# Optimization experiments

Hardware: AMD Instinct MI355X
Metric: run time of the kernel (lower is better)

Reference implementation:

```python
import jax, jax.numpy as jnp
import numpy as np

B, S, D = 4, 2048, 768
LN_EPS = 1e-12


def setup_inputs() -> dict:
    key = jax.random.key(0)
    k0, k1, k2, k3 = jax.random.split(key, 4)
    scale = 1.0 / np.sqrt(D).astype(np.float32)
    return {
        "hidden_states": jax.random.normal(k0, (B, S, D), jnp.float32),
        "attention_mask": jnp.ones((B, 1, S, S), jnp.int32),
        "prior_n_attn": jax.random.uniform(k1, (B, S, S), jnp.float32),
        "ln_w": jnp.ones((D,), jnp.float32),
        "ln_b": jnp.zeros((D,), jnp.float32),
        "wq": jax.random.normal(k2, (D, D), jnp.float32) * scale,
        "bq": jnp.zeros((D,), jnp.float32),
        "wk": jax.random.normal(k3, (D, D), jnp.float32) * scale,
        "bk": jnp.zeros((D,), jnp.float32),
    }


def reference(hidden_states, attention_mask, prior_n_attn, ln_w, ln_b, wq, bq, wk, bk):
    _, S_, D_ = hidden_states.shape
    # LayerNorm (biased variance, as torch.nn.LayerNorm)
    mu = hidden_states.mean(-1, keepdims=True)
    var = ((hidden_states - mu) ** 2).mean(-1, keepdims=True)
    h = (hidden_states - mu) / jnp.sqrt(var + LN_EPS) * ln_w + ln_b

    a = jnp.eye(S_, k=1, dtype=jnp.int32)      # superdiagonal
    bI = jnp.eye(S_, dtype=jnp.int32)          # diagonal
    c = jnp.eye(S_, k=-1, dtype=jnp.int32)     # subdiagonal
    tri = jnp.triu(jnp.ones((S_, S_), jnp.float32))

    # mask & (a + c): band of width 1 off the diagonal; then squeeze dim 1
    mask = (attention_mask.astype(jnp.int32) & (a + c))[:, 0]  # [B,S,S]

    q = h @ wq + bq
    k = h @ wk + bk
    scores = jnp.einsum("bsd,btd->bst", q, k) / D_
    scores = jnp.where(mask == 0, -jnp.inf, scores)
    n = jnp.nan_to_num(jax.nn.softmax(scores, axis=-1))
    n = jnp.sqrt(n * jnp.swapaxes(n, -2, -1) + 1e-9)
    n = prior_n_attn + (1.0 - prior_n_attn) * n

    # keep only the superdiagonal of log(n + 1e-9); zero elsewhere
    logm = jnp.log(n + 1e-9) * a.astype(n.dtype)
    # prefix-sum via triangular matmuls (same math as torch source)
    t = logm @ tri                                   # [B,S,S]
    g = jnp.exp(jnp.einsum("ij,bjk->bik", tri, t))   # [B,S,S]
    su = tri - bI.astype(tri.dtype)                  # strictly-upper indicator
    g = g * su                                       # masked_fill((tri-b)==0, 0)
    diag_part = jnp.where(bI == 0, 1e-9, n)          # n.masked_fill(b==0, 1e-9)
    g = g + jnp.swapaxes(g, -2, -1) + diag_part
    return (g, n)
```

## Files before the change

kernel.cpp:

```cpp
#include <hip/hip_runtime.h>
#include <hip/hip_bf16.h>
#include <math.h>
#include <stdint.h>

#define BB 4
#define SS 2048
#define DD 768
#define MM (BB*SS)

typedef __attribute__((ext_vector_type(4))) float  f32x4;
typedef __attribute__((ext_vector_type(8))) __bf16 bf16x8;
typedef __attribute__((ext_vector_type(4))) __bf16 bf16x4;

#define AS1 __attribute__((address_space(1)))
#define AS3 __attribute__((address_space(3)))

__global__ __launch_bounds__(256) void combined_kernel(
        const float* __restrict__ x, const float* __restrict__ lw,
        const float* __restrict__ lb, const float* __restrict__ wq,
        const float* __restrict__ wk, const float* __restrict__ bq,
        const float* __restrict__ bk, const int* __restrict__ att,
        const float* __restrict__ prior, __bf16* __restrict__ G,
        float* __restrict__ u, float* __restrict__ v, float* __restrict__ cb,
        __bf16* __restrict__ h, int* __restrict__ fl, float* __restrict__ prsup,
        float* __restrict__ du_g, float* __restrict__ dn_g, float* __restrict__ w_g) {
    __shared__ __attribute__((aligned(16))) __bf16 As[64][32];
    __shared__ __attribute__((aligned(16))) __bf16 Bs[64][32];
    const int bid = blockIdx.x;
    if (bid >= 2577) {
        const int idx = (bid - 2577) * 256 + threadIdx.x;
        const int b = idx >> 11, s = idx & 2047;
        const bool au = (s < SS - 1) && ((att[((size_t)b * SS + s) * SS + (s + 1)] & 1) != 0);
        const bool ad = (s > 0)      && ((att[((size_t)b * SS + s) * SS + (s - 1)] & 1) != 0);
        fl[idx] = (au ? 1 : 0) | (ad ? 2 : 0);
        if (s < SS - 1)
            prsup[idx] = prior[((size_t)b * SS + s) * SS + s + 1];
        du_g[idx] = 0.f; dn_g[idx] = 0.f; w_g[idx] = 0.f;
        return;
    }
    if (bid >= 529) {
        const int row = (bid - 529) * 4 + (threadIdx.x >> 6);
        const int lane = threadIdx.x & 63;
        const float* xr = x + (size_t)row * DD + lane * 12;
        f32x4 a0 = *(const f32x4*)(xr), a1 = *(const f32x4*)(xr + 4), a2 = *(const f32x4*)(xr + 8);
        float xs[12];
#pragma unroll
        for (int c = 0; c < 4; c++) { xs[c] = a0[c]; xs[4 + c] = a1[c]; xs[8 + c] = a2[c]; }
        float s = 0.f, ss = 0.f;
#pragma unroll
        for (int c = 0; c < 12; c++) { s += xs[c]; ss += xs[c] * xs[c]; }
#pragma unroll
        for (int o = 1; o < 64; o <<= 1) { s += __shfl_xor(s, o); ss += __shfl_xor(ss, o); }
        const float mu = s * (1.0f / DD);
        const float var = ss * (1.0f / DD) - mu * mu;
        const float rstd = 1.0f / sqrtf(var + 1e-12f);
        const float* wp = lw + lane * 12; const float* bp = lb + lane * 12;
        f32x4 w0 = *(const f32x4*)(wp), w1 = *(const f32x4*)(wp + 4), w2 = *(const f32x4*)(wp + 8);
        f32x4 b0 = *(const f32x4*)(bp), b1 = *(const f32x4*)(bp + 4), b2 = *(const f32x4*)(bp + 8);
        bf16x4 o0, o1, o2;
#pragma unroll
        for (int c = 0; c < 4; c++) {
            o0[c] = (__bf16)((xs[c]     - mu) * rstd * w0[c] + b0[c]);
            o1[c] = (__bf16)((xs[4 + c] - mu) * rstd * w1[c] + b1[c]);
            o2[c] = (__bf16)((xs[8 + c] - mu) * rstd * w2[c] + b2[c]);
        }
        __bf16* hr = h + (size_t)row * DD + lane * 12;
        *(bf16x4*)(hr) = o0; *(bf16x4*)(hr + 4) = o1; *(bf16x4*)(hr + 8) = o2;
        return;
    }
    if (bid >= 144) {
        const int id = bid - 144;
        const int lane = threadIdx.x & 63, wv_ = threadIdx.x >> 6;
        if (id == 384) {
            if (wv_ != 0) return;
            float s = 0.f;
#pragma unroll
            for (int m = 0; m < 12; m++) s += bq[lane + 64 * m] * bk[lane + 64 * m];
#pragma unroll
            for (int o = 1; o < 64; o <<= 1) s += __shfl_xor(s, o);
            if (lane == 0) cb[0] = s;
            return;
        }
        const bool isU = id < 192;
        const int row = (isU ? id : id - 192) * 4 + wv_;
        const float* W = isU ? wq : wk;
        const float* bvec = isU ? bk : bq;
        const float* wr_ = W + (size_t)row * DD;
        float s = 0.f;
#pragma unroll
        for (int m = 0; m < 12; m++) s += wr_[lane + 64 * m] * bvec[lane + 64 * m];
#pragma unroll
        for (int o = 1; o < 64; o <<= 1) s += __shfl_xor(s, o);
        if (lane == 0) (isU ? u : v)[row] = s;
        return;
    }
    const int m0 = (bid % 12) * 64;
    const int n0 = (bid / 12) * 64;
    const int t = threadIdx.x;
    const int wave = t >> 6, lane = t & 63;
    const int wr = wave >> 1, wc = wave & 1;
    const int srow = t >> 2, scol = (t & 3) * 8;
    f32x4 acc[2][2] = {};

    for (int k0 = 0; k0 < DD; k0 += 32) {
        const float* ga = wq + (size_t)(m0 + srow) * DD + k0 + scol;
        const float* gb = wk + (size_t)(n0 + srow) * DD + k0 + scol;
        f32x4 a0 = *(const f32x4*)(ga), a1 = *(const f32x4*)(ga + 4);
        f32x4 b0 = *(const f32x4*)(gb), b1 = *(const f32x4*)(gb + 4);
        bf16x8 av, bv;
#pragma unroll
        for (int c = 0; c < 4; c++) {
            av[c] = (__bf16)a0[c]; av[4 + c] = (__bf16)a1[c];
            bv[c] = (__bf16)b0[c]; bv[4 + c] = (__bf16)b1[c];
        }
        __syncthreads();
        *(bf16x8*)&As[srow][scol] = av;
        *(bf16x8*)&Bs[srow][scol] = bv;
        __syncthreads();
        const int r = lane & 15, ko = (lane >> 4) << 3;
        bf16x8 af[2], bvf[2];
#pragma unroll
        for (int i = 0; i < 2; i++) af[i]  = *(const bf16x8*)&As[wr * 32 + i * 16 + r][ko];
#pragma unroll
        for (int j = 0; j < 2; j++) bvf[j] = *(const bf16x8*)&Bs[wc * 32 + j * 16 + r][ko];
#pragma unroll
        for (int i = 0; i < 2; i++)
#pragma unroll
            for (int j = 0; j < 2; j++)
                acc[i][j] = __builtin_amdgcn_mfma_f32_16x16x32_bf16(af[i], bvf[j], acc[i][j], 0, 0, 0);
    }
#pragma unroll
    for (int i = 0; i < 2; i++) {
        const int mm = m0 + wr * 32 + i * 16 + (lane >> 4) * 4;
#pragma unroll
        for (int j = 0; j < 2; j++) {
            const int nn = n0 + wc * 32 + j * 16 + (lane & 15);
#pragma unroll
            for (int rr = 0; rr < 4; rr++)
                G[(size_t)(mm + rr) * DD + nn] = (__bf16)acc[i][j][rr];
        }
    }
}

__global__ __launch_bounds__(256) void rgemm_kernel(const __bf16* __restrict__ A,
        const __bf16* __restrict__ Bt, const float* __restrict__ u,
        const float* __restrict__ v, float* __restrict__ du_g,
        float* __restrict__ dn_g, float* __restrict__ w_g) {
    __shared__ __attribute__((aligned(16))) __bf16 As[64 * 32];
    __shared__ __attribute__((aligned(16))) __bf16 Bs[128 * 32];
    const int bid = blockIdx.x;
    const int mt = bid & 127, nt = bid >> 7;
    const int m0 = mt * 64, n0 = nt * 128;
    const int t = threadIdx.x;
    const int wave = t >> 6, lane = t & 63;
    const int wr = wave >> 1, wc = wave & 1;
    f32x4 acc[2][4] = {};

    char* asb = (char*)As;
    char* bsb = (char*)Bs;
    const int rloc = lane >> 2;
    const int slot = lane & 3;
    const int rA = wave * 16 + rloc;
    const int csw = (slot ^ ((rA >> 1) & 3)) << 3;

    for (int k0 = 0; k0 < DD; k0 += 32) {
        const __bf16* ga  = A  + (size_t)(m0 + rA) * DD + k0 + csw;
        const __bf16* gb0 = Bt + (size_t)(n0 + rA) * DD + k0 + csw;
        const __bf16* gb1 = gb0 + (size_t)64 * DD;
        __builtin_amdgcn_global_load_lds((const AS1 void*)(ga),  (AS3 void*)(asb + wave * 1024),        16, 0, 0);
        __builtin_amdgcn_global_load_lds((const AS1 void*)(gb0), (AS3 void*)(bsb + wave * 1024),        16, 0, 0);
        __builtin_amdgcn_global_load_lds((const AS1 void*)(gb1), (AS3 void*)(bsb + 4096 + wave * 1024), 16, 0, 0);
        __syncthreads();
        const int r = lane & 15, ks = lane >> 4;
        bf16x8 af[2], bvf[4];
#pragma unroll
        for (int i = 0; i < 2; i++) {
            const int R = wr * 32 + i * 16 + r;
            af[i] = *(const bf16x8*)&As[R * 32 + ((ks ^ ((R >> 1) & 3)) << 3)];
        }
#pragma unroll
        for (int j = 0; j < 4; j++) {
            const int R = wc * 64 + j * 16 + r;
            bvf[j] = *(const bf16x8*)&Bs[R * 32 + ((ks ^ ((R >> 1) & 3)) << 3)];
        }
#pragma unroll
        for (int i = 0; i < 2; i++)
#pragma unroll
            for (int j = 0; j < 4; j++)
                acc[i][j] = __builtin_amdgcn_mfma_f32_16x16x32_bf16(af[i], bvf[j], acc[i][j], 0, 0, 0);
        __syncthreads();
    }
    int colg[4]; float ub[4], vb[4];
#pragma unroll
    for (int j = 0; j < 4; j++) {
        colg[j] = n0 + wc * 64 + j * 16 + (lane & 15);
        ub[j] = u[colg[j]];
        vb[j] = v[colg[j]];
    }
#pragma unroll
    for (int i = 0; i < 2; i++) {
#pragma unroll
        for (int rr = 0; rr < 4; rr++) {
            const int row = m0 + wr * 32 + i * 16 + (lane >> 4) * 4 + rr;
            const int rm = (row == 0) ? 0 : row - 1;
            const int rp = (row == MM - 1) ? MM - 1 : row + 1;
            const __bf16* hm = A + (size_t)rm * DD;
            const __bf16* hz = A + (size_t)row * DD;
            const __bf16* hp = A + (size_t)rp * DD;
            float dua = 0.f, dna = 0.f, wa = 0.f;
#pragma unroll
            for (int j = 0; j < 4; j++) {
                const float Rv = acc[i][j][rr] + ub[j];
                dua += Rv * (float)hm[colg[j]];
                dna += Rv * (float)hp[colg[j]];
                wa  += vb[j] * (float)hz[colg[j]];
            }
#pragma unroll
            for (int o = 1; o < 16; o <<= 1) {
                dua += __shfl_xor(dua, o);
                dna += __shfl_xor(dna, o);
                wa  += __shfl_xor(wa, o);
            }
            if ((lane & 15) == 0) {
                atomicAdd(&du_g[row], dua);
                atomicAdd(&dn_g[row], dna);
                atomicAdd(&w_g[row], wa);
            }
        }
    }
}

__global__ __launch_bounds__(256) void scan_kernel(const float* __restrict__ du_g,
        const float* __restrict__ dn_g, const float* __restrict__ w_g,
        const float* __restrict__ cbp, const int* __restrict__ fl_i,
        const float* __restrict__ prsup,
        float* __restrict__ nb, double* __restrict__ P2) {
    const int b = blockIdx.x;
    const int t = threadIdx.x;
    __shared__ float du_s[SS], dn_s[SS], w_s[SS], sh_pd[SS];
    __shared__ double warr[256];
    for (int x = t; x < SS; x += 256) {
        du_s[x] = du_g[b * SS + x];
        dn_s[x] = dn_g[b * SS + x];
        w_s[x]  = w_g[b * SS + x];
    }
    __syncthreads();
    const float cb = cbp[0];
    float pu_r[8];
#pragma unroll
    for (int e = 0; e < 8; e++) {
        const int s = t * 8 + e;
        const int fl = fl_i[b * SS + s];
        const bool au = fl & 1, ad = fl & 2;
        float puv = 0.f, pdv = 0.f;
        if (au || ad) {
            const float eu = au ? (du_s[s + 1] + w_s[s + 1] + cb) * (1.0f / DD) : 0.f;
            const float ed = ad ? (dn_s[s - 1] + w_s[s - 1] + cb) * (1.0f / DD) : 0.f;
            float mx = au ? eu : ed;
            if (au && ad) mx = fmaxf(eu, ed);
            const float zu = au ? expf(eu - mx) : 0.f;
            const float zd = ad ? expf(ed - mx) : 0.f;
            const float iz = 1.f / (zu + zd);
            puv = zu * iz; pdv = zd * iz;
        }
        pu_r[e] = puv;
        sh_pd[s] = pdv;
    }
    __syncthreads();
    double L[8];
    double mysum = 0.0;
#pragma unroll
    for (int e = 0; e < 8; e++) {
        const int s = t * 8 + e;
        double Lv = 0.0;
        float nbv = 0.f;
        if (s < SS - 1) {
            nbv = sqrtf(pu_r[e] * sh_pd[s + 1] + 1e-9f);
            const float pr = prsup[b * SS + s];
            const float nsup = pr + (1.f - pr) * nbv;
            Lv = (double)log2f(nsup + 1e-9f);
        }
        nb[b * SS + s] = nbv;
        L[e] = Lv; mysum += Lv;
    }
    warr[t] = mysum;
    __syncthreads();
    for (int o = 1; o < 256; o <<= 1) {
        double vv = 0.0;
        if (t >= o) vv = warr[t - o];
        __syncthreads();
        if (t >= o) warr[t] += vv;
        __syncthreads();
    }
    double run = warr[t] - mysum;
#pragma unroll
    for (int e = 0; e < 8; e++) {
        P2[(size_t)b * SS + t * 8 + e] = run;
        run += L[e];
    }
}

__global__ __launch_bounds__(256) void out_kernel(const float* __restrict__ prior,
        const float* __restrict__ nb, const double* __restrict__ P2,
        float* __restrict__ gout, float* __restrict__ nout) {
    const size_t t8 = (size_t)blockIdx.x * 256 + threadIdx.x;
    const int b = (int)(t8 >> 19);
    const size_t off = t8 << 3;
    const size_t r = off & ((1u << 22) - 1);
    const int i  = (int)(r >> 11);
    const int k0 = (int)(r & 2047);
    const f32x4 p0 = *(const f32x4*)(prior + off);
    const f32x4 p1 = *(const f32x4*)(prior + off + 4);
    const double* Pb = P2 + ((size_t)b << 11);
    const double Pi = Pb[i];
    const float* nbb = nb + ((size_t)b << 11);
    f32x4 g0, g1, n0, n1;
#pragma unroll
    for (int c = 0; c < 8; c++) {
        const int k = k0 + c;
        const float pr = (c < 4) ? p0[c] : p1[c - 4];
        float vv = 3.16227766016838e-5f;
        if (k == i + 1)      vv = nbb[i];
        else if (k == i - 1) vv = nbb[k];
        const float nval = pr + (1.f - pr) * vv;
        float g;
        if (k == i) {
            g = nval;
        } else {
            const double Pk = Pb[k];
            const double dd = (k > i) ? (Pk - Pi) : (Pi - Pk);
            g = exp2f((float)dd) + 1e-9f;
        }
        if (c < 4) { g0[c] = g; n0[c] = nval; }
        else       { g1[c - 4] = g; n1[c - 4] = nval; }
    }
    *(f32x4*)(gout + off)     = g0;
    *(f32x4*)(gout + off + 4) = g1;
    *(f32x4*)(nout + off)     = n0;
    *(f32x4*)(nout + off + 4) = n1;
}

extern "C" void kernel_launch(void* const* d_in, const int* in_sizes, int n_in,
                              void* d_out, int out_size, void* d_ws, size_t ws_size,
                              hipStream_t stream) {
    const float* hs    = (const float*)d_in[0];
    const int*   att   = (const int*)d_in[1];
    const float* prior = (const float*)d_in[2];
    const float* ln_w  = (const float*)d_in[3];
    const float* ln_b  = (const float*)d_in[4];
    const float* wq    = (const float*)d_in[5];
    const float* bq    = (const float*)d_in[6];
    const float* wk    = (const float*)d_in[7];
    const float* bk    = (const float*)d_in[8];

    float* gout = (float*)d_out;
    float* nout = gout + (size_t)BB * SS * SS;

    char* ws = (char*)d_ws;
    __bf16* h     = (__bf16*)(ws);
    __bf16* G     = (__bf16*)(ws + 12582912);
    float*  u     = (float*) (ws + 13762560);
    float*  v     = (float*) (ws + 13765632);
    float*  cbp   = (float*) (ws + 13768704);
    int*    fl    = (int*)   (ws + 13768960);
    float*  prsup = (float*) (ws + 13801728);
    float*  du_g  = (float*) (ws + 13834496);
    float*  dn_g  = (float*) (ws + 13867264);
    float*  w_g   = (float*) (ws + 13900032);
    float*  nbuf  = (float*) (ws + 13932800);
    double* P2    = (double*)(ws + 13965568);

    combined_kernel<<<dim3(2609), dim3(256), 0, stream>>>(hs, ln_w, ln_b, wq, wk, bq, bk,
                                                          att, prior, G, u, v, cbp, h, fl, prsup,
                                                          du_g, dn_g, w_g);
    rgemm_kernel<<<dim3(768), dim3(256), 0, stream>>>(h, G, u, v, du_g, dn_g, w_g);
    scan_kernel<<<dim3(BB), dim3(256), 0, stream>>>(du_g, dn_g, w_g, cbp, fl, prsup, nbuf, P2);
    out_kernel<<<dim3((BB * SS * SS / 8) / 256), dim3(256), 0, stream>>>(prior, nbuf, P2, gout, nout);
}
```

Baseline: 97.39 us.

## Fuse four kernel launches into one cooperative persistent kernel with grid syncs

Adds a cooperative mega-kernel of 512 blocks that runs the LayerNorm/weight-product prep, the h·G reduction GEMM, the per-batch scan and the output fill in sequence, separated by grid.sync(). It also adds a host-side occupancy check that falls back to the old four-launch path. The intent is to remove three kernel launch gaps and their tail effects. In exchange, the fixed 512-block grid may underuse the GPU in the large output phase, and the scan phase leaves most blocks idle during a grid barrier. The host also now makes device attribute and occupancy queries on every call.

```diff
diff --git a/kernel.cpp b/kernel.cpp
--- a/kernel.cpp
+++ b/kernel.cpp
@@ -1,5 +1,6 @@
 #include <hip/hip_runtime.h>
 #include <hip/hip_bf16.h>
+#include <hip/hip_cooperative_groups.h>
 #include <math.h>
 #include <stdint.h>
 
@@ -7,6 +8,7 @@
 #define SS 2048
 #define DD 768
 #define MM (BB*SS)
+#define MGRID 512
 
 typedef __attribute__((ext_vector_type(4))) float  f32x4;
 typedef __attribute__((ext_vector_type(8))) __bf16 bf16x8;
@@ -14,6 +16,330 @@
 
 #define AS1 __attribute__((address_space(1)))
 #define AS3 __attribute__((address_space(3)))
+
+namespace cg = cooperative_groups;
+
+__global__ __launch_bounds__(256, 2) void mega_kernel(
+        const float* __restrict__ x, const float* __restrict__ lw,
+        const float* __restrict__ lb, const float* __restrict__ wq,
+        const float* __restrict__ bq, const float* __restrict__ wk,
+        const float* __restrict__ bk, const int* __restrict__ att,
+        const float* __restrict__ prior,
+        __bf16* __restrict__ G, float* __restrict__ u, float* __restrict__ v,
+        float* __restrict__ cbp, __bf16* __restrict__ h, int* __restrict__ fl,
+        float* __restrict__ prsup, float* __restrict__ du_g,
+        float* __restrict__ dn_g, float* __restrict__ w_g,
+        float* __restrict__ nbuf, double* __restrict__ P2,
+        float* __restrict__ gout, float* __restrict__ nout) {
+    __shared__ __attribute__((aligned(16))) union {
+        struct { __bf16 As[128 * 32]; __bf16 Bs[96 * 32]; } g;
+        struct { __bf16 As[64][32]; __bf16 Bs[64][32]; } g0;
+        struct { float du[SS], dn[SS], w[SS], pd[SS]; double warr[256]; } s;
+    } sm;
+    cg::grid_group grid = cg::this_grid();
+    const int bid = blockIdx.x;
+    const int t = threadIdx.x;
+    const int wave = t >> 6, lane = t & 63;
+
+    {
+#pragma unroll
+        for (int rr = 0; rr < 4; rr++) {
+            const int row = bid * 16 + wave * 4 + rr;
+            const float* xr = x + (size_t)row * DD + lane * 12;
+            f32x4 a0 = *(const f32x4*)(xr), a1 = *(const f32x4*)(xr + 4), a2 = *(const f32x4*)(xr + 8);
+            float xs[12];
+#pragma unroll
+            for (int c = 0; c < 4; c++) { xs[c] = a0[c]; xs[4 + c] = a1[c]; xs[8 + c] = a2[c]; }
+            float s = 0.f, ss = 0.f;
+#pragma unroll
+            for (int c = 0; c < 12; c++) { s += xs[c]; ss += xs[c] * xs[c]; }
+#pragma unroll
+            for (int o = 1; o < 64; o <<= 1) { s += __shfl_xor(s, o); ss += __shfl_xor(ss, o); }
+            const float mu = s * (1.0f / DD);
+            const float var = ss * (1.0f / DD) - mu * mu;
+            const float rstd = 1.0f / sqrtf(var + 1e-12f);
+            const float* wp = lw + lane * 12; const float* bp = lb + lane * 12;
+            f32x4 w0 = *(const f32x4*)(wp), w1 = *(const f32x4*)(wp + 4), w2 = *(const f32x4*)(wp + 8);
+            f32x4 b0 = *(const f32x4*)(bp), b1 = *(const f32x4*)(bp + 4), b2 = *(const f32x4*)(bp + 8);
+            bf16x4 o0, o1, o2;
+#pragma unroll
+            for (int c = 0; c < 4; c++) {
+                o0[c] = (__bf16)((xs[c]     - mu) * rstd * w0[c] + b0[c]);
+                o1[c] = (__bf16)((xs[4 + c] - mu) * rstd * w1[c] + b1[c]);
+                o2[c] = (__bf16)((xs[8 + c] - mu) * rstd * w2[c] + b2[c]);
+            }
+            __bf16* hr = h + (size_t)row * DD + lane * 12;
+            *(bf16x4*)(hr) = o0; *(bf16x4*)(hr + 4) = o1; *(bf16x4*)(hr + 8) = o2;
+        }
+        if (bid < 144) {
+            const int m0 = (bid % 12) * 64;
+            const int n0 = (bid / 12) * 64;
+            const int wr = wave >> 1, wc = wave & 1;
+            const int srow = t >> 2, scol = (t & 3) * 8;
+            f32x4 acc[2][2] = {};
+            for (int k0 = 0; k0 < DD; k0 += 32) {
+                const float* ga = wq + (size_t)(m0 + srow) * DD + k0 + scol;
+                const float* gb = wk + (size_t)(n0 + srow) * DD + k0 + scol;
+                f32x4 a0 = *(const f32x4*)(ga), a1 = *(const f32x4*)(ga + 4);
+                f32x4 b0 = *(const f32x4*)(gb), b1 = *(const f32x4*)(gb + 4);
+                bf16x8 av, bv;
+#pragma unroll
+                for (int c = 0; c < 4; c++) {
+                    av[c] = (__bf16)a0[c]; av[4 + c] = (__bf16)a1[c];
+                    bv[c] = (__bf16)b0[c]; bv[4 + c] = (__bf16)b1[c];
+                }
+                __syncthreads();
+                *(bf16x8*)&sm.g0.As[srow][scol] = av;
+                *(bf16x8*)&sm.g0.Bs[srow][scol] = bv;
+                __syncthreads();
+                const int r = lane & 15, ko = (lane >> 4) << 3;
+                bf16x8 af[2], bvf[2];
+#pragma unroll
+                for (int i = 0; i < 2; i++) af[i]  = *(const bf16x8*)&sm.g0.As[wr * 32 + i * 16 + r][ko];
+#pragma unroll
+                for (int j = 0; j < 2; j++) bvf[j] = *(const bf16x8*)&sm.g0.Bs[wc * 32 + j * 16 + r][ko];
+#pragma unroll
+                for (int i = 0; i < 2; i++)
+#pragma unroll
+                    for (int j = 0; j < 2; j++)
+                        acc[i][j] = __builtin_amdgcn_mfma_f32_16x16x32_bf16(af[i], bvf[j], acc[i][j], 0, 0, 0);
+            }
+#pragma unroll
+            for (int i = 0; i < 2; i++) {
+                const int mm = m0 + wr * 32 + i * 16 + (lane >> 4) * 4;
+#pragma unroll
+                for (int j = 0; j < 2; j++) {
+                    const int nn = n0 + wc * 32 + j * 16 + (lane & 15);
+#pragma unroll
+                    for (int rr = 0; rr < 4; rr++)
+                        G[(size_t)(mm + rr) * DD + nn] = (__bf16)acc[i][j][rr];
+                }
+            }
+        } else if (bid < 337) {
+            const int base = (bid - 144) * 2;
+#pragma unroll 1
+            for (int q = 0; q < 2; q++) {
+                const int id = base + q;
+                if (id > 384) break;
+                if (id == 384) {
+                    if (wave == 0) {
+                        float s = 0.f;
+#pragma unroll
+                        for (int m = 0; m < 12; m++) s += bq[lane + 64 * m] * bk[lane + 64 * m];
+#pragma unroll
+                        for (int o = 1; o < 64; o <<= 1) s += __shfl_xor(s, o);
+                        if (lane == 0) cbp[0] = s;
+                    }
+                } else {
+                    const bool isU = id < 192;
+                    const int row = (isU ? id : id - 192) * 4 + wave;
+                    const float* W = isU ? wq : wk;
+                    const float* bvec = isU ? bk : bq;
+                    const float* wr_ = W + (size_t)row * DD;
+                    float s = 0.f;
+#pragma unroll
+                    for (int m = 0; m < 12; m++) s += wr_[lane + 64 * m] * bvec[lane + 64 * m];
+#pragma unroll
+                    for (int o = 1; o < 64; o <<= 1) s += __shfl_xor(s, o);
+                    if (lane == 0) (isU ? u : v)[row] = s;
+                }
+            }
+        } else if (bid >= 480) {
+            const int idx = (bid - 480) * 256 + t;
+            const int b = idx >> 11, s = idx & 2047;
+            const bool au = (s < SS - 1) && ((att[((size_t)b * SS + s) * SS + (s + 1)] & 1) != 0);
+            const bool ad = (s > 0)      && ((att[((size_t)b * SS + s) * SS + (s - 1)] & 1) != 0);
+            fl[idx] = (au ? 1 : 0) | (ad ? 2 : 0);
+            if (s < SS - 1)
+                prsup[idx] = prior[((size_t)b * SS + s) * SS + s + 1];
+            du_g[idx] = 0.f; dn_g[idx] = 0.f; w_g[idx] = 0.f;
+        }
+    }
+    grid.sync();
+    {
+        const int mt = bid & 63, nt = bid >> 6;
+        const int m0 = mt * 128, n0 = nt * 96;
+        const int wr = wave >> 1, wc = wave & 1;
+        f32x4 acc[4][3] = {};
+        char* asb = (char*)sm.g.As;
+        char* bsb = (char*)sm.g.Bs;
+        const int rgrp = lane >> 2;
+        const int slot = lane & 3;
+#pragma unroll 1
+        for (int k0 = 0; k0 < DD; k0 += 32) {
+#pragma unroll
+            for (int i2 = 0; i2 < 2; i2++) {
+                const int j = wave * 2 + i2;
+                const int R = j * 16 + rgrp;
+                const int csw = (slot ^ ((R >> 1) & 3)) << 3;
+                __builtin_amdgcn_global_load_lds((const AS1 void*)(h + (size_t)(m0 + R) * DD + k0 + csw),
+                                                 (AS3 void*)(asb + j * 1024), 16, 0, 0);
+                if (j < 6)
+                    __builtin_amdgcn_global_load_lds((const AS1 void*)(G + (size_t)(n0 + R) * DD + k0 + csw),
+                                                     (AS3 void*)(bsb + j * 1024), 16, 0, 0);
+            }
+            __syncthreads();
+            const int r = lane & 15, ks = lane >> 4;
+            bf16x8 af[4], bvf[3];
+#pragma unroll
+            for (int i = 0; i < 4; i++) {
+                const int R = wr * 64 + i * 16 + r;
+                af[i] = *(const bf16x8*)&sm.g.As[R * 32 + ((ks ^ ((R >> 1) & 3)) << 3)];
+            }
+#pragma unroll
+            for (int j = 0; j < 3; j++) {
+                const int R = wc * 48 + j * 16 + r;
+                bvf[j] = *(const bf16x8*)&sm.g.Bs[R * 32 + ((ks ^ ((R >> 1) & 3)) << 3)];
+            }
+#pragma unroll
+            for (int i = 0; i < 4; i++)
+#pragma unroll
+                for (int j = 0; j < 3; j++)
+                    acc[i][j] = __builtin_amdgcn_mfma_f32_16x16x32_bf16(af[i], bvf[j], acc[i][j], 0, 0, 0);
+            __syncthreads();
+        }
+        int colg[3]; float ub[3], vb2[3];
+#pragma unroll
+        for (int j = 0; j < 3; j++) {
+            colg[j] = n0 + wc * 48 + j * 16 + (lane & 15);
+            ub[j] = u[colg[j]];
+            vb2[j] = v[colg[j]];
+        }
+#pragma unroll
+        for (int i = 0; i < 4; i++) {
+#pragma unroll
+            for (int rr = 0; rr < 4; rr++) {
+                const int row = m0 + wr * 64 + i * 16 + (lane >> 4) * 4 + rr;
+                const int rm = (row == 0) ? 0 : row - 1;
+                const int rp = (row == MM - 1) ? MM - 1 : row + 1;
+                const __bf16* hm = h + (size_t)rm * DD;
+                const __bf16* hz = h + (size_t)row * DD;
+                const __bf16* hp = h + (size_t)rp * DD;
+                float dua = 0.f, dna = 0.f, wa = 0.f;
+#pragma unroll
+                for (int j = 0; j < 3; j++) {
+                    const float Rv = acc[i][j][rr] + ub[j];
+                    dua += Rv * (float)hm[colg[j]];
+                    dna += Rv * (float)hp[colg[j]];
+                    wa  += vb2[j] * (float)hz[colg[j]];
+                }
+#pragma unroll
+                for (int o = 1; o < 16; o <<= 1) {
+                    dua += __shfl_xor(dua, o);
+                    dna += __shfl_xor(dna, o);
+                    wa  += __shfl_xor(wa, o);
+                }
+                if ((lane & 15) == 0) {
+                    atomicAdd(&du_g[row], dua);
+                    atomicAdd(&dn_g[row], dna);
+                    atomicAdd(&w_g[row], wa);
+                }
+            }
+        }
+    }
+    grid.sync();
+    if (bid < BB) {
+        const int b = bid;
+        for (int xx = t; xx < SS; xx += 256) {
+            sm.s.du[xx] = du_g[b * SS + xx];
+            sm.s.dn[xx] = dn_g[b * SS + xx];
+            sm.s.w[xx]  = w_g[b * SS + xx];
+        }
+        __syncthreads();
+        const float cb = cbp[0];
+        float pu_r[8];
+#pragma unroll
+        for (int e = 0; e < 8; e++) {
+            const int s = t * 8 + e;
+            const int flg = fl[b * SS + s];
+            const bool au = flg & 1, ad = flg & 2;
+            float puv = 0.f, pdv = 0.f;
+            if (au || ad) {
+                const float eu = au ? (sm.s.du[s + 1] + sm.s.w[s + 1] + cb) * (1.0f / DD) : 0.f;
+                const float ed = ad ? (sm.s.dn[s - 1] + sm.s.w[s - 1] + cb) * (1.0f / DD) : 0.f;
+                float mx = au ? eu : ed;
+                if (au && ad) mx = fmaxf(eu, ed);
+                const float zu = au ? expf(eu - mx) : 0.f;
+                const float zd = ad ? expf(ed - mx) : 0.f;
+                const float iz = 1.f / (zu + zd);
+                puv = zu * iz; pdv = zd * iz;
+            }
+            pu_r[e] = puv;
+            sm.s.pd[s] = pdv;
+        }
+        __syncthreads();
+        double L[8];
+        double mysum = 0.0;
+#pragma unroll
+        for (int e = 0; e < 8; e++) {
+            const int s = t * 8 + e;
+            double Lv = 0.0;
+            float nbv = 0.f;
+            if (s < SS - 1) {
+                nbv = sqrtf(pu_r[e] * sm.s.pd[s + 1] + 1e-9f);
+                const float pr = prsup[b * SS + s];
+                const float nsup = pr + (1.f - pr) * nbv;
+                Lv = (double)log2f(nsup + 1e-9f);
+            }
+            nbuf[b * SS + s] = nbv;
+            L[e] = Lv; mysum += Lv;
+        }
+        sm.s.warr[t] = mysum;
+        __syncthreads();
+        for (int o = 1; o < 256; o <<= 1) {
+            double vv = 0.0;
+            if (t >= o) vv = sm.s.warr[t - o];
+            __syncthreads();
+            if (t >= o) sm.s.warr[t] += vv;
+            __syncthreads();
+        }
+        double run = sm.s.warr[t] - mysum;
+#pragma unroll
+        for (int e = 0; e < 8; e++) {
+            P2[(size_t)b * SS + t * 8 + e] = run;
+            run += L[e];
+        }
+    }
+    grid.sync();
+#pragma unroll 1
+    for (int vb = bid; vb < 8192; vb += MGRID) {
+        const size_t t8 = (size_t)vb * 256 + t;
+        const int b = (int)(t8 >> 19);
+        const size_t off = t8 << 3;
+        const size_t rr_ = off & ((1u << 22) - 1);
+        const int i  = (int)(rr_ >> 11);
+        const int k0 = (int)(rr_ & 2047);
+        const f32x4 p0 = *(const f32x4*)(prior + off);
+        const f32x4 p1 = *(const f32x4*)(prior + off + 4);
+        const double* Pb = P2 + ((size_t)b << 11);
+        const double Pi = Pb[i];
+        const float* nbb = nbuf + ((size_t)b << 11);
+        f32x4 g0, g1, n0v, n1v;
+#pragma unroll
+        for (int c = 0; c < 8; c++) {
+            const int k = k0 + c;
+            const float pr = (c < 4) ? p0[c] : p1[c - 4];
+            float vv = 3.16227766016838e-5f;
+            if (k == i + 1)      vv = nbb[i];
+            else if (k == i - 1) vv = nbb[k];
+            const float nval = pr + (1.f - pr) * vv;
+            float g;
+            if (k == i) {
+                g = nval;
+            } else {
+                const double Pk = Pb[k];
+                const double dd = (k > i) ? (Pk - Pi) : (Pi - Pk);
+                g = exp2f((float)dd) + 1e-9f;
+            }
+            if (c < 4) { g0[c] = g; n0v[c] = nval; }
+            else       { g1[c - 4] = g; n1v[c - 4] = nval; }
+        }
+        *(f32x4*)(gout + off)     = g0;
+        *(f32x4*)(gout + off + 4) = g1;
+        *(f32x4*)(nout + off)     = n0v;
+        *(f32x4*)(nout + off + 4) = n1v;
+    }
+}
 
 __global__ __launch_bounds__(256) void combined_kernel(
         const float* __restrict__ x, const float* __restrict__ lw,
@@ -370,6 +696,30 @@
     float*  nbuf  = (float*) (ws + 13932800);
     double* P2    = (double*)(ws + 13965568);
 
+    bool useCoop = false;
+    {
+        int dev = 0;
+        if (hipGetDevice(&dev) == hipSuccess) {
+            int coop = 0, nCU = 0, maxBlk = 0;
+            hipDeviceGetAttribute(&coop, hipDeviceAttributeCooperativeLaunch, dev);
+            hipDeviceGetAttribute(&nCU, hipDeviceAttributeMultiprocessorCount, dev);
+            hipError_t oe = hipOccupancyMaxActiveBlocksPerMultiprocessor(&maxBlk, mega_kernel, 256, 0);
+            useCoop = (coop != 0) && (oe == hipSuccess) && ((long)maxBlk * nCU >= MGRID);
+        }
+    }
+    if (useCoop) {
+        void* args[] = {
+            (void*)&hs, (void*)&ln_w, (void*)&ln_b, (void*)&wq, (void*)&bq,
+            (void*)&wk, (void*)&bk, (void*)&att, (void*)&prior,
+            (void*)&G, (void*)&u, (void*)&v, (void*)&cbp, (void*)&h, (void*)&fl,
+            (void*)&prsup, (void*)&du_g, (void*)&dn_g, (void*)&w_g,
+            (void*)&nbuf, (void*)&P2, (void*)&gout, (void*)&nout
+        };
+        if (hipLaunchCooperativeKernel((const void*)mega_kernel, dim3(MGRID), dim3(256),
+                                       args, 0, stream) == hipSuccess)
+            return;
+        (void)hipGetLastError();
+    }
     combined_kernel<<<dim3(2609), dim3(256), 0, stream>>>(hs, ln_w, ln_b, wq, wk, bq, bk,
                                                           att, prior, G, u, v, cbp, h, fl, prsup,
                                                           du_g, dn_g, w_g);
```

Result: slower. 292.2 us (+200.0%).

## Fuse per-batch scan into output kernel, recomputing prefix sums per row block

Applied to the files above, without the earlier changes.

Removes the separate 4-block scan kernel and its global nb/P2 buffers. Each of the 8192 output blocks now recomputes the softmax band, the log terms and a 256-thread double-precision prefix scan for its batch, then writes one row of g and n. This drops a serial, low-occupancy launch and the round trip through the global P2 buffer. In exchange it repeats the scan 2048 times per batch, adding double-precision work, many syncthreads and extra reads of du/dn/w/prsup in every block.

```diff
diff --git a/kernel.cpp b/kernel.cpp
--- a/kernel.cpp
+++ b/kernel.cpp
@@ -230,32 +230,33 @@
     }
 }
 
-__global__ __launch_bounds__(256) void scan_kernel(const float* __restrict__ du_g,
-        const float* __restrict__ dn_g, const float* __restrict__ w_g,
-        const float* __restrict__ cbp, const int* __restrict__ fl_i,
-        const float* __restrict__ prsup,
-        float* __restrict__ nb, double* __restrict__ P2) {
-    const int b = blockIdx.x;
+__global__ __launch_bounds__(256) void out_kernel(const float* __restrict__ prior,
+        const float* __restrict__ du_g, const float* __restrict__ dn_g,
+        const float* __restrict__ w_g, const float* __restrict__ cbp,
+        const int* __restrict__ fl_i, const float* __restrict__ prsup,
+        float* __restrict__ gout, float* __restrict__ nout) {
+    __shared__ float sh_pd[SS];
+    __shared__ double warr[256];
+    __shared__ double sh_P2i;
+    __shared__ float sh_nbi, sh_nbim1;
+    const int bid = blockIdx.x;
+    const int b = bid >> 11;
+    const int i = bid & 2047;
     const int t = threadIdx.x;
-    __shared__ float du_s[SS], dn_s[SS], w_s[SS], sh_pd[SS];
-    __shared__ double warr[256];
-    for (int x = t; x < SS; x += 256) {
-        du_s[x] = du_g[b * SS + x];
-        dn_s[x] = dn_g[b * SS + x];
-        w_s[x]  = w_g[b * SS + x];
-    }
-    __syncthreads();
     const float cb = cbp[0];
+
     float pu_r[8];
 #pragma unroll
     for (int e = 0; e < 8; e++) {
         const int s = t * 8 + e;
-        const int fl = fl_i[b * SS + s];
-        const bool au = fl & 1, ad = fl & 2;
+        const int idx = b * SS + s;
+        const int flg = fl_i[idx];
+        const bool au = flg & 1, ad = flg & 2;
         float puv = 0.f, pdv = 0.f;
         if (au || ad) {
-            const float eu = au ? (du_s[s + 1] + w_s[s + 1] + cb) * (1.0f / DD) : 0.f;
-            const float ed = ad ? (dn_s[s - 1] + w_s[s - 1] + cb) * (1.0f / DD) : 0.f;
+            float eu = 0.f, ed = 0.f;
+            if (au) eu = (du_g[idx + 1] + w_g[idx + 1] + cb) * (1.0f / DD);
+            if (ad) ed = (dn_g[idx - 1] + w_g[idx - 1] + cb) * (1.0f / DD);
             float mx = au ? eu : ed;
             if (au && ad) mx = fmaxf(eu, ed);
             const float zu = au ? expf(eu - mx) : 0.f;
@@ -280,7 +281,8 @@
             const float nsup = pr + (1.f - pr) * nbv;
             Lv = (double)log2f(nsup + 1e-9f);
         }
-        nb[b * SS + s] = nbv;
+        if (s == i)     sh_nbi   = nbv;
+        if (s == i - 1) sh_nbim1 = nbv;
         L[e] = Lv; mysum += Lv;
     }
     warr[t] = mysum;
@@ -293,42 +295,33 @@
         __syncthreads();
     }
     double run = warr[t] - mysum;
+    double P2loc[8];
 #pragma unroll
     for (int e = 0; e < 8; e++) {
-        P2[(size_t)b * SS + t * 8 + e] = run;
+        P2loc[e] = run;
+        if (t * 8 + e == i) sh_P2i = run;
         run += L[e];
     }
-}
-
-__global__ __launch_bounds__(256) void out_kernel(const float* __restrict__ prior,
-        const float* __restrict__ nb, const double* __restrict__ P2,
-        float* __restrict__ gout, float* __restrict__ nout) {
-    const size_t t8 = (size_t)blockIdx.x * 256 + threadIdx.x;
-    const int b = (int)(t8 >> 19);
-    const size_t off = t8 << 3;
-    const size_t r = off & ((1u << 22) - 1);
-    const int i  = (int)(r >> 11);
-    const int k0 = (int)(r & 2047);
+    __syncthreads();
+    const double Pi = sh_P2i;
+    const float nbi = sh_nbi, nbim1 = sh_nbim1;
+    const size_t off = ((size_t)bid << 11) + (size_t)t * 8;
     const f32x4 p0 = *(const f32x4*)(prior + off);
     const f32x4 p1 = *(const f32x4*)(prior + off + 4);
-    const double* Pb = P2 + ((size_t)b << 11);
-    const double Pi = Pb[i];
-    const float* nbb = nb + ((size_t)b << 11);
     f32x4 g0, g1, n0, n1;
 #pragma unroll
     for (int c = 0; c < 8; c++) {
-        const int k = k0 + c;
+        const int k = t * 8 + c;
         const float pr = (c < 4) ? p0[c] : p1[c - 4];
         float vv = 3.16227766016838e-5f;
-        if (k == i + 1)      vv = nbb[i];
-        else if (k == i - 1) vv = nbb[k];
+        if (k == i + 1)      vv = nbi;
+        else if (k == i - 1) vv = nbim1;
         const float nval = pr + (1.f - pr) * vv;
         float g;
         if (k == i) {
             g = nval;
         } else {
-            const double Pk = Pb[k];
-            const double dd = (k > i) ? (Pk - Pi) : (Pi - Pk);
+            const double dd = (k > i) ? (P2loc[c] - Pi) : (Pi - P2loc[c]);
             g = exp2f((float)dd) + 1e-9f;
         }
         if (c < 4) { g0[c] = g; n0[c] = nval; }
@@ -367,13 +360,10 @@
     float*  du_g  = (float*) (ws + 13834496);
     float*  dn_g  = (float*) (ws + 13867264);
     float*  w_g   = (float*) (ws + 13900032);
-    float*  nbuf  = (float*) (ws + 13932800);
-    double* P2    = (double*)(ws + 13965568);
 
     combined_kernel<<<dim3(2609), dim3(256), 0, stream>>>(hs, ln_w, ln_b, wq, wk, bq, bk,
                                                           att, prior, G, u, v, cbp, h, fl, prsup,
                                                           du_g, dn_g, w_g);
     rgemm_kernel<<<dim3(768), dim3(256), 0, stream>>>(h, G, u, v, du_g, dn_g, w_g);
-    scan_kernel<<<dim3(BB), dim3(256), 0, stream>>>(du_g, dn_g, w_g, cbp, fl, prsup, nbuf, P2);
-    out_kernel<<<dim3((BB * SS * SS / 8) / 256), dim3(256), 0, stream>>>(prior, nbuf, P2, gout, nout);
+    out_kernel<<<dim3(MM), dim3(256), 0, stream>>>(prior, du_g, dn_g, w_g, cbp, fl, prsup, gout, nout);
 }
```

Result: slower. 238.3 us (+144.7%).
